# Kernel tuning notes

Measured on AMD Instinct MI355X. Metric: run time of the kernel, lower is better.

The kernel has to match this reference:

```python
import jax, jax.numpy as jnp
import numpy as np

B, N, DIM = 4, 16384, 256
H, D, G = 8, 64, 32  # heads, dim_head, slice_num; inner = H*D = 512


def setup_inputs() -> dict:
    key = jax.random.key(0)
    ks = jax.random.split(key, 12)
    inner = H * D
    s = lambda fan_in: 1.0 / np.sqrt(fan_in)
    inp = {
        "x": jax.random.normal(ks[0], (B, N, DIM), jnp.float32),
        # weights stored (in, out) so forward is x @ W + b
        "Wfx": jax.random.uniform(ks[1], (DIM, inner), jnp.float32, -s(DIM), s(DIM)),
        "bfx": jnp.zeros((inner,), jnp.float32),
        "Wx": jax.random.uniform(ks[2], (DIM, inner), jnp.float32, -s(DIM), s(DIM)),
        "bx": jnp.zeros((inner,), jnp.float32),
        "Wslice": jnp.linalg.qr(jax.random.normal(ks[3], (D, G), jnp.float32))[0],  # orthogonal init
        "bslice": jnp.zeros((G,), jnp.float32),
        "temperature": jnp.full((1, H, 1, 1), 0.5, jnp.float32),
        "Wq": jax.random.uniform(ks[4], (D, D), jnp.float32, -s(D), s(D)),
        "Wk": jax.random.uniform(ks[5], (D, D), jnp.float32, -s(D), s(D)),
        "Wv": jax.random.uniform(ks[6], (D, D), jnp.float32, -s(D), s(D)),
        "Wout": jax.random.uniform(ks[7], (inner, DIM), jnp.float32, -s(inner), s(inner)),
        "bout": jnp.zeros((DIM,), jnp.float32),
    }
    return inp


def reference(x, Wfx, bfx, Wx, bx, Wslice, bslice, temperature, Wq, Wk, Wv, Wout, bout):
    b, n, _ = x.shape
    # projections -> [B, H, N, D]
    fx_mid = (x @ Wfx + bfx).reshape(b, n, H, D).transpose(0, 2, 1, 3)
    x_mid = (x @ Wx + bx).reshape(b, n, H, D).transpose(0, 2, 1, 3)
    # soft slice assignment: [B, H, N, G]
    slice_logits = (x_mid @ Wslice + bslice) / temperature
    slice_weights = jax.nn.softmax(slice_logits, axis=-1)
    slice_norm = slice_weights.sum(axis=2)  # [B, H, G]
    # soft pooling to G slice tokens: [B, H, G, D]
    slice_token = jnp.einsum("bhnd,bhng->bhgd", fx_mid, slice_weights)
    slice_token = slice_token / (slice_norm[..., None] + 1e-5)
    # tiny attention over G tokens
    q = slice_token @ Wq
    k = slice_token @ Wk
    v = slice_token @ Wv
    scores = jnp.einsum("bhgd,bhkd->bhgk", q, k) / jnp.sqrt(jnp.asarray(D, q.dtype))
    attn = jax.nn.softmax(scores, axis=-1)
    out_slice = jnp.einsum("bhgk,bhkd->bhgd", attn, v)
    # scatter back to N points: [B, H, N, D] -> [B, N, H*D]
    out_x = jnp.einsum("bhgd,bhng->bhnd", out_slice, slice_weights)
    out_x = out_x.transpose(0, 2, 1, 3).reshape(b, n, H * D)
    return out_x @ Wout + bout
```

## Files before the change

### kernel.cpp

```cpp
#include <hip/hip_runtime.h>


typedef unsigned short u16;
typedef __attribute__((ext_vector_type(8))) unsigned short ushort8v;
typedef __attribute__((ext_vector_type(4))) unsigned short ushort4v;
typedef __attribute__((ext_vector_type(8))) short short8v;
typedef __attribute__((ext_vector_type(4))) float f32x4;

constexpr int Nc = 16384;
constexpr int BNc = 65536;

__device__ inline float b2f(u16 v) {
    union { unsigned int u; float f; } t; t.u = ((unsigned int)v) << 16; return t.f;
}
__device__ inline u16 f2b(float f) {
    union { float f; unsigned int u; } t; t.f = f;
    unsigned int u = t.u;
    return (u16)((u + 0x7fffu + ((u >> 16) & 1u)) >> 16);
}

__global__ __launch_bounds__(256) void k0_fold(
    const float* __restrict__ Wx, const float* __restrict__ Wslice,
    const float* __restrict__ bx, const float* __restrict__ bslice,
    u16* __restrict__ WxsT, float* __restrict__ bxs)
{
    int blk = blockIdx.x, tid = threadIdx.x;
    int h = tid >> 5, g = tid & 31;
    if (blk < 256) {
        int k = blk;
        float acc = 0.f;
        for (int d = 0; d < 64; d++)
            acc += Wx[k * 512 + h * 64 + d] * Wslice[d * 32 + g];
        WxsT[tid * 256 + k] = f2b(acc);
    } else {
        float acc = 0.f;
        for (int d = 0; d < 64; d++)
            acc += bx[h * 64 + d] * Wslice[d * 32 + g];
        bxs[tid] = acc + bslice[g];
    }
}

__global__ __launch_bounds__(256) void kprep_wfx(const float* __restrict__ Wfx,
                                                 u16* __restrict__ WfxT)
{
    int n = blockIdx.x, k = threadIdx.x;
    WfxT[n * 256 + k] = f2b(Wfx[k * 512 + n]);
}

template <int MODE, int NT>
__global__ __launch_bounds__(256, 2) void kgemm(
    const void* __restrict__ Ap, const u16* __restrict__ Bt,
    const float* __restrict__ bias, const float* __restrict__ temp,
    void* __restrict__ O1, u16* __restrict__ O2)
{
    constexpr int Kd = 256;
    __shared__ u16 Asl[4][64][8];
    __shared__ u16 Bsl[NT * 16][4][8];
    int tid = threadIdx.x;
    int wave = tid >> 6, lane = tid & 63;
    int lm = lane & 15, quad = lane >> 4;
    int row0 = blockIdx.x * 64;
    int sm = tid >> 2, skb = tid & 3;
    const u16* BtB = Bt;
    if (MODE == 2) BtB += (size_t)(row0 >> 14) * 65536;
    f32x4 acc[NT] = {};

    for (int k0 = 0; k0 < Kd; k0 += 32) {
        if (MODE < 2) {
            const float* A32 = (const float*)Ap;
            const f32x4* src = (const f32x4*)(A32 + (size_t)(row0 + sm) * Kd + k0 + skb * 8);
            f32x4 v0 = src[0], v1 = src[1];
            ushort8v o;
#pragma unroll
            for (int j = 0; j < 4; j++) { o[j] = f2b(v0[j]); o[4 + j] = f2b(v1[j]); }
            *(ushort8v*)&Asl[skb][sm][0] = o;
        } else {
            const u16* A16 = (const u16*)Ap;
            *(ushort8v*)&Asl[skb][sm][0] =
                *(const ushort8v*)(A16 + (size_t)(row0 + sm) * Kd + k0 + skb * 8);
        }
#pragma unroll
        for (int i = 0; i < NT / 4; i++) {
            int e = i * 256 + tid;
            int sn = e >> 2, sk = e & 3;
            *(ushort8v*)&Bsl[sn][sk][0] =
                *(const ushort8v*)(BtB + (size_t)sn * Kd + k0 + sk * 8);
        }
        __syncthreads();
        short8v af = *(short8v*)&Asl[quad][wave * 16 + lm][0];
#pragma unroll
        for (int nt = 0; nt < NT; nt++) {
            short8v bf = *(short8v*)&Bsl[nt * 16 + lm][quad][0];
            acc[nt] = __builtin_amdgcn_mfma_f32_16x16x32_bf16(af, bf, acc[nt], 0, 0, 0);
        }
        __syncthreads();
    }

    if (MODE == 0) {
        u16* fxT = (u16*)O1;
        int nbase = row0 + wave * 16 + quad * 4;
#pragma unroll
        for (int nt = 0; nt < NT; nt++) {
            int c = nt * 16 + lm;
            float bv = bias[c];
            ushort4v o;
#pragma unroll
            for (int r = 0; r < 4; r++) o[r] = f2b(acc[nt][r] + bv);
            *(ushort4v*)(fxT + (size_t)c * 65536 + nbase) = o;
        }
    } else if (MODE == 1) {
        int b = row0 >> 14;
        int nlbase = (row0 & 16383) + wave * 16 + quad * 4;
        u16* swb = (u16*)O1;
#pragma unroll
        for (int h = 0; h < 8; h++) {
            float it = 1.0f / temp[h];
            float bv0 = bias[h * 32 + lm];
            float bv1 = bias[h * 32 + 16 + lm];
            ushort4v p0, p1;
#pragma unroll
            for (int r = 0; r < 4; r++) {
                float v0 = (acc[2 * h][r] + bv0) * it;
                float v1 = (acc[2 * h + 1][r] + bv1) * it;
                float m = fmaxf(v0, v1);
                m = fmaxf(m, __shfl_xor(m, 1));
                m = fmaxf(m, __shfl_xor(m, 2));
                m = fmaxf(m, __shfl_xor(m, 4));
                m = fmaxf(m, __shfl_xor(m, 8));
                float e0 = __expf(v0 - m), e1 = __expf(v1 - m);
                float s = e0 + e1;
                s += __shfl_xor(s, 1);
                s += __shfl_xor(s, 2);
                s += __shfl_xor(s, 4);
                s += __shfl_xor(s, 8);
                float rs = 1.0f / s;
                float w0 = e0 * rs, w1 = e1 * rs;
                int row = row0 + wave * 16 + quad * 4 + r;
                swb[(size_t)row * 256 + h * 32 + lm] = f2b(w0);
                swb[(size_t)row * 256 + h * 32 + 16 + lm] = f2b(w1);
                p0[r] = f2b(w0); p1[r] = f2b(w1);
            }
            size_t gbase = (size_t)((b * 8 + h) * 32);
            *(ushort4v*)(O2 + (gbase + lm) * 16384 + nlbase) = p0;
            *(ushort4v*)(O2 + (gbase + 16 + lm) * 16384 + nlbase) = p1;
        }
    } else {
        float* out = (float*)O1;
#pragma unroll
        for (int nt = 0; nt < NT; nt++) {
            int c = nt * 16 + lm;
            float bv = bias[c];
#pragma unroll
            for (int r = 0; r < 4; r++)
                out[(size_t)(row0 + wave * 16 + quad * 4 + r) * 256 + c] = acc[nt][r] + bv;
        }
    }
}

__global__ __launch_bounds__(256) void k4_token_mfma(
    const u16* __restrict__ swT, const u16* __restrict__ fxT,
    float* __restrict__ token_part, float* __restrict__ norm_part)
{
    int bh = blockIdx.x, ky = blockIdx.y;
    int b = bh >> 3, h = bh & 7;
    int tid = threadIdx.x, wave = tid >> 6, lane = tid & 63;
    int lm = lane & 15, quad = lane >> 4;
    int mt = wave & 1, dp = wave >> 1;
    const u16* Ar = swT + ((size_t)(bh * 32 + mt * 16 + lm)) * 16384 + ky * 512 + quad * 8;
    const u16* Br0 = fxT + ((size_t)(h * 64 + dp * 32 + lm)) * 65536
                     + (size_t)b * 16384 + ky * 512 + quad * 8;
    const u16* Br1 = Br0 + (size_t)16 * 65536;
    f32x4 acc0 = {}, acc1 = {};
    float nacc = 0.f;
#pragma unroll
    for (int kk = 0; kk < 16; kk++) {
        short8v af = *(const short8v*)(Ar + kk * 32);
        short8v b0 = *(const short8v*)(Br0 + kk * 32);
        short8v b1 = *(const short8v*)(Br1 + kk * 32);
        acc0 = __builtin_amdgcn_mfma_f32_16x16x32_bf16(af, b0, acc0, 0, 0, 0);
        acc1 = __builtin_amdgcn_mfma_f32_16x16x32_bf16(af, b1, acc1, 0, 0, 0);
        if (dp == 0) {
            ushort8v au = (ushort8v&)af;
#pragma unroll
            for (int j = 0; j < 8; j++) nacc += b2f(au[j]);
        }
    }
    float* tp = token_part + ((size_t)(ky * 32 + bh)) * 2048;
#pragma unroll
    for (int r = 0; r < 4; r++) {
        int g = mt * 16 + quad * 4 + r;
        tp[g * 64 + dp * 32 + lm] = acc0[r];
        tp[g * 64 + dp * 32 + 16 + lm] = acc1[r];
    }
    if (dp == 0) {
        nacc += __shfl_xor(nacc, 16);
        nacc += __shfl_xor(nacc, 32);
        if (lane < 16)
            norm_part[(ky * 32 + bh) * 32 + mt * 16 + lm] = nacc;
    }
}

__global__ __launch_bounds__(256) void k4b_reduce(
    const float* __restrict__ tp, const float* __restrict__ np,
    float* __restrict__ tl)
{
    int t = blockIdx.x * 256 + threadIdx.x;
    int bh = t >> 11, e = t & 2047, g = e >> 6;
    float ts = 0.f, ns = 0.f;
    for (int ch = 0; ch < 32; ch++) {
        ts += tp[((size_t)(ch * 32 + bh)) * 2048 + e];
        ns += np[(ch * 32 + bh) * 32 + g];
    }
    tl[t] = ts / (ns + 1e-5f);
}

__global__ __launch_bounds__(256) void k5_attn(
    const float* __restrict__ tlg,
    const float* __restrict__ Wq, const float* __restrict__ Wk, const float* __restrict__ Wv,
    float* __restrict__ out_slice)
{
    __shared__ float tl[32][64];
    __shared__ float ql[32][64], kl[32][64], vl[32][64];
    __shared__ float sl[32][33];
    int bh = blockIdx.x, tid = threadIdx.x;
    const float* tk = tlg + (size_t)bh * 2048;

#pragma unroll
    for (int j = 0; j < 8; j++) {
        int idx = j * 256 + tid;
        tl[idx >> 6][idx & 63] = tk[idx];
    }
    __syncthreads();
#pragma unroll
    for (int j = 0; j < 8; j++) {
        int idx = j * 256 + tid;
        int g = idx >> 6, d = idx & 63;
        float aq = 0.f, ak = 0.f, av = 0.f;
        for (int e = 0; e < 64; e++) {
            float t = tl[g][e];
            aq += t * Wq[e * 64 + d];
            ak += t * Wk[e * 64 + d];
            av += t * Wv[e * 64 + d];
        }
        ql[g][d] = aq; kl[g][d] = ak; vl[g][d] = av;
    }
    __syncthreads();
#pragma unroll
    for (int j = 0; j < 4; j++) {
        int idx = j * 256 + tid;
        int gq = idx >> 5, gk = idx & 31;
        float s = 0.f;
        for (int d = 0; d < 64; d++) s += ql[gq][d] * kl[gk][d];
        sl[gq][gk] = s * 0.125f;
    }
    __syncthreads();
    if (tid < 32) {
        float m = -1e30f;
        for (int k2 = 0; k2 < 32; k2++) m = fmaxf(m, sl[tid][k2]);
        float s = 0.f;
        for (int k2 = 0; k2 < 32; k2++) { float e = __expf(sl[tid][k2] - m); sl[tid][k2] = e; s += e; }
        float r = 1.0f / s;
        for (int k2 = 0; k2 < 32; k2++) sl[tid][k2] *= r;
    }
    __syncthreads();
#pragma unroll
    for (int j = 0; j < 8; j++) {
        int idx = j * 256 + tid;
        int g = idx >> 6, d = idx & 63;
        float a = 0.f;
        for (int k2 = 0; k2 < 32; k2++) a += sl[g][k2] * vl[k2][d];
        out_slice[(size_t)bh * 2048 + idx] = a;
    }
}

__global__ __launch_bounds__(256) void kZ(
    const float* __restrict__ os, const float* __restrict__ Wout,
    u16* __restrict__ ZT)
{
    int b = blockIdx.x, cb = blockIdx.y;
    int t = threadIdx.x;
    int c = cb * 16 + (t & 15), kq = t >> 4;
    for (int k = kq * 16; k < kq * 16 + 16; k++) {
        int h = k >> 5, g = k & 31;
        const float* osr = os + ((size_t)(b * 8 + h)) * 2048 + g * 64;
        float acc = 0.f;
        for (int d = 0; d < 64; d++)
            acc += osr[d] * Wout[(h * 64 + d) * 256 + c];
        ZT[(size_t)b * 65536 + c * 256 + k] = f2b(acc);
    }
}

extern "C" void kernel_launch(void* const* d_in, const int* in_sizes, int n_in,
                              void* d_out, int out_size, void* d_ws, size_t ws_size,
                              hipStream_t stream)
{
    const float* x      = (const float*)d_in[0];
    const float* Wfx    = (const float*)d_in[1];
    const float* bfx    = (const float*)d_in[2];
    const float* Wx     = (const float*)d_in[3];
    const float* bx     = (const float*)d_in[4];
    const float* Wslice = (const float*)d_in[5];
    const float* bslice = (const float*)d_in[6];
    const float* temp   = (const float*)d_in[7];
    const float* Wq     = (const float*)d_in[8];
    const float* Wk     = (const float*)d_in[9];
    const float* Wv     = (const float*)d_in[10];
    const float* Wout   = (const float*)d_in[11];
    const float* bout   = (const float*)d_in[12];

    char* ws = (char*)d_ws;
    size_t off = 0;
    auto alloc = [&](size_t bytes) {
        void* p = ws + off;
        off = (off + bytes + 255) & ~(size_t)255;
        return p;
    };
    u16*   fxT   = (u16*)  alloc((size_t)512 * BNc * 2);
    u16*   swb   = (u16*)  alloc((size_t)BNc * 256 * 2);
    u16*   swT   = (u16*)  alloc((size_t)1024 * Nc * 2);
    float* tp    = (float*)alloc((size_t)1024 * 2048 * 4);
    float* np    = (float*)alloc(32768 * 4);
    float* tl    = (float*)alloc(65536 * 4);
    float* osl   = (float*)alloc(65536 * 4);
    u16*   ZT    = (u16*)  alloc(4 * 65536 * 2);
    u16*   WfxT  = (u16*)  alloc(512 * 256 * 2);
    u16*   WxsT  = (u16*)  alloc(256 * 256 * 2);
    float* bxs   = (float*)alloc(256 * 4);

    k0_fold<<<257, 256, 0, stream>>>(Wx, Wslice, bx, bslice, WxsT, bxs);
    kprep_wfx<<<512, 256, 0, stream>>>(Wfx, WfxT);

    kgemm<0, 32><<<1024, 256, 0, stream>>>(x, WfxT, bfx, nullptr, fxT, nullptr);

    kgemm<1, 16><<<1024, 256, 0, stream>>>(x, WxsT, bxs, temp, swb, swT);

    k4_token_mfma<<<dim3(32, 32), 256, 0, stream>>>(swT, fxT, tp, np);
    k4b_reduce<<<256, 256, 0, stream>>>(tp, np, tl);
    k5_attn<<<32, 256, 0, stream>>>(tl, Wq, Wk, Wv, osl);
    kZ<<<dim3(4, 16), 256, 0, stream>>>(osl, Wout, ZT);

    kgemm<2, 16><<<1024, 256, 0, stream>>>(swb, ZT, bout, nullptr, d_out, nullptr);
}
```

Measured before the change: 351.8 us.

## Fuse fx and slice projections into one GEMM, drop LDS staging

Concatenates the Wfx and folded Wx·Wslice weights into one bf16 matrix. A single kernel now reads x once and computes both the fx projection and the slice-softmax weights, where two separate GEMMs each read x before. Both the projection and output GEMMs now load operand fragments straight from global memory into registers, prefetching the next A chunk and dropping shared-memory staging and the __syncthreads barriers. The cost is higher register pressure (24 accumulators per wave), uneven work between the two wave columns (one only writes fx, the other also does the softmax), and repeated uncoalesced B loads that now rely on cache.

```diff
diff --git a/kernel.cpp b/kernel.cpp
--- a/kernel.cpp
+++ b/kernel.cpp
@@ -47,81 +47,72 @@
     WfxT[n * 256 + k] = f2b(Wfx[k * 512 + n]);
 }
 
-template <int MODE, int NT>
-__global__ __launch_bounds__(256, 2) void kgemm(
-    const void* __restrict__ Ap, const u16* __restrict__ Bt,
-    const float* __restrict__ bias, const float* __restrict__ temp,
-    void* __restrict__ O1, u16* __restrict__ O2)
-{
-    constexpr int Kd = 256;
-    __shared__ u16 Asl[4][64][8];
-    __shared__ u16 Bsl[NT * 16][4][8];
+__global__ __launch_bounds__(256, 3) void kproj(
+    const float* __restrict__ x, const u16* __restrict__ Ball,
+    const float* __restrict__ bfx, const float* __restrict__ bxs,
+    const float* __restrict__ temp,
+    u16* __restrict__ fxT, u16* __restrict__ swb, u16* __restrict__ swT)
+{
     int tid = threadIdx.x;
     int wave = tid >> 6, lane = tid & 63;
     int lm = lane & 15, quad = lane >> 4;
-    int row0 = blockIdx.x * 64;
-    int sm = tid >> 2, skb = tid & 3;
-    const u16* BtB = Bt;
-    if (MODE == 2) BtB += (size_t)(row0 >> 14) * 65536;
-    f32x4 acc[NT] = {};
-
-    for (int k0 = 0; k0 < Kd; k0 += 32) {
-        if (MODE < 2) {
-            const float* A32 = (const float*)Ap;
-            const f32x4* src = (const f32x4*)(A32 + (size_t)(row0 + sm) * Kd + k0 + skb * 8);
-            f32x4 v0 = src[0], v1 = src[1];
-            ushort8v o;
-#pragma unroll
-            for (int j = 0; j < 4; j++) { o[j] = f2b(v0[j]); o[4 + j] = f2b(v1[j]); }
-            *(ushort8v*)&Asl[skb][sm][0] = o;
-        } else {
-            const u16* A16 = (const u16*)Ap;
-            *(ushort8v*)&Asl[skb][sm][0] =
-                *(const ushort8v*)(A16 + (size_t)(row0 + sm) * Kd + k0 + skb * 8);
-        }
-#pragma unroll
-        for (int i = 0; i < NT / 4; i++) {
-            int e = i * 256 + tid;
-            int sn = e >> 2, sk = e & 3;
-            *(ushort8v*)&Bsl[sn][sk][0] =
-                *(const ushort8v*)(BtB + (size_t)sn * Kd + k0 + sk * 8);
-        }
-        __syncthreads();
-        short8v af = *(short8v*)&Asl[quad][wave * 16 + lm][0];
-#pragma unroll
-        for (int nt = 0; nt < NT; nt++) {
-            short8v bf = *(short8v*)&Bsl[nt * 16 + lm][quad][0];
-            acc[nt] = __builtin_amdgcn_mfma_f32_16x16x32_bf16(af, bf, acc[nt], 0, 0, 0);
-        }
-        __syncthreads();
-    }
-
-    if (MODE == 0) {
-        u16* fxT = (u16*)O1;
-        int nbase = row0 + wave * 16 + quad * 4;
-#pragma unroll
-        for (int nt = 0; nt < NT; nt++) {
-            int c = nt * 16 + lm;
-            float bv = bias[c];
+    int wr = wave & 1, wc = wave >> 1;
+    int row0 = blockIdx.x * 32;
+    int arow = row0 + wr * 16 + lm;
+
+    const float* Aptr = x + (size_t)arow * 256 + quad * 8;
+    const u16*   Bl   = Ball + (size_t)(wc * 384 + lm) * 256 + quad * 8;
+
+    f32x4 acc[24] = {};
+
+    f32x4 a0 = *(const f32x4*)(Aptr);
+    f32x4 a1 = *(const f32x4*)(Aptr + 4);
+
+    for (int k0 = 0; k0 < 256; k0 += 32) {
+        ushort8v au;
+#pragma unroll
+        for (int j = 0; j < 4; j++) { au[j] = f2b(a0[j]); au[4 + j] = f2b(a1[j]); }
+        short8v af = (short8v&)au;
+        if (k0 < 224) {
+            a0 = *(const f32x4*)(Aptr + k0 + 32);
+            a1 = *(const f32x4*)(Aptr + k0 + 36);
+        }
+#pragma unroll
+        for (int j = 0; j < 24; j++) {
+            short8v bf = *(const short8v*)(Bl + (size_t)j * 4096 + k0);
+            acc[j] = __builtin_amdgcn_mfma_f32_16x16x32_bf16(af, bf, acc[j], 0, 0, 0);
+        }
+    }
+
+    int nbase = row0 + wr * 16 + quad * 4;
+    int nfx = wc ? 8 : 24;
+#pragma unroll
+    for (int j = 0; j < 24; j++) {
+        if (j < nfx) {
+            int c = (wc * 24 + j) * 16 + lm;
+            float bv = bfx[c];
             ushort4v o;
 #pragma unroll
-            for (int r = 0; r < 4; r++) o[r] = f2b(acc[nt][r] + bv);
+            for (int r = 0; r < 4; r++) o[r] = f2b(acc[j][r] + bv);
             *(ushort4v*)(fxT + (size_t)c * 65536 + nbase) = o;
         }
-    } else if (MODE == 1) {
+    }
+
+    if (wc == 1) {
         int b = row0 >> 14;
-        int nlbase = (row0 & 16383) + wave * 16 + quad * 4;
-        u16* swb = (u16*)O1;
+        int nlbase = (row0 & 16383) + wr * 16 + quad * 4;
 #pragma unroll
         for (int h = 0; h < 8; h++) {
             float it = 1.0f / temp[h];
-            float bv0 = bias[h * 32 + lm];
-            float bv1 = bias[h * 32 + 16 + lm];
+            float bv0 = bxs[h * 32 + lm];
+            float bv1 = bxs[h * 32 + 16 + lm];
+            f32x4 A0 = acc[8 + 2 * h];
+            f32x4 A1 = acc[9 + 2 * h];
             ushort4v p0, p1;
 #pragma unroll
             for (int r = 0; r < 4; r++) {
-                float v0 = (acc[2 * h][r] + bv0) * it;
-                float v1 = (acc[2 * h + 1][r] + bv1) * it;
+                float v0 = (A0[r] + bv0) * it;
+                float v1 = (A1[r] + bv1) * it;
                 float m = fmaxf(v0, v1);
                 m = fmaxf(m, __shfl_xor(m, 1));
                 m = fmaxf(m, __shfl_xor(m, 2));
@@ -135,25 +126,48 @@
                 s += __shfl_xor(s, 8);
                 float rs = 1.0f / s;
                 float w0 = e0 * rs, w1 = e1 * rs;
-                int row = row0 + wave * 16 + quad * 4 + r;
+                int row = row0 + wr * 16 + quad * 4 + r;
                 swb[(size_t)row * 256 + h * 32 + lm] = f2b(w0);
                 swb[(size_t)row * 256 + h * 32 + 16 + lm] = f2b(w1);
                 p0[r] = f2b(w0); p1[r] = f2b(w1);
             }
             size_t gbase = (size_t)((b * 8 + h) * 32);
-            *(ushort4v*)(O2 + (gbase + lm) * 16384 + nlbase) = p0;
-            *(ushort4v*)(O2 + (gbase + 16 + lm) * 16384 + nlbase) = p1;
-        }
-    } else {
-        float* out = (float*)O1;
-#pragma unroll
-        for (int nt = 0; nt < NT; nt++) {
-            int c = nt * 16 + lm;
-            float bv = bias[c];
-#pragma unroll
-            for (int r = 0; r < 4; r++)
-                out[(size_t)(row0 + wave * 16 + quad * 4 + r) * 256 + c] = acc[nt][r] + bv;
-        }
+            *(ushort4v*)(swT + (gbase + lm) * 16384 + nlbase) = p0;
+            *(ushort4v*)(swT + (gbase + 16 + lm) * 16384 + nlbase) = p1;
+        }
+    }
+}
+
+__global__ __launch_bounds__(256, 3) void kout(
+    const u16* __restrict__ swb, const u16* __restrict__ ZT,
+    const float* __restrict__ bout, float* __restrict__ out)
+{
+    int tid = threadIdx.x;
+    int wave = tid >> 6, lane = tid & 63;
+    int lm = lane & 15, quad = lane >> 4;
+    int row0 = blockIdx.x * 64;
+
+    const u16* Abase = swb + (size_t)(row0 + wave * 16 + lm) * 256 + quad * 8;
+    const u16* Bl    = ZT + (size_t)(row0 >> 14) * 65536 + (size_t)lm * 256 + quad * 8;
+
+    f32x4 acc[16] = {};
+    short8v af = *(const short8v*)(Abase);
+    for (int k0 = 0; k0 < 256; k0 += 32) {
+        short8v a_cur = af;
+        if (k0 < 224) af = *(const short8v*)(Abase + k0 + 32);
+#pragma unroll
+        for (int j = 0; j < 16; j++) {
+            short8v bf = *(const short8v*)(Bl + (size_t)j * 4096 + k0);
+            acc[j] = __builtin_amdgcn_mfma_f32_16x16x32_bf16(a_cur, bf, acc[j], 0, 0, 0);
+        }
+    }
+#pragma unroll
+    for (int j = 0; j < 16; j++) {
+        int c = j * 16 + lm;
+        float bv = bout[c];
+#pragma unroll
+        for (int r = 0; r < 4; r++)
+            out[(size_t)(row0 + wave * 16 + quad * 4 + r) * 256 + c] = acc[j][r] + bv;
     }
 }
 
@@ -323,21 +337,21 @@
     float* tl    = (float*)alloc(65536 * 4);
     float* osl   = (float*)alloc(65536 * 4);
     u16*   ZT    = (u16*)  alloc(4 * 65536 * 2);
-    u16*   WfxT  = (u16*)  alloc(512 * 256 * 2);
-    u16*   WxsT  = (u16*)  alloc(256 * 256 * 2);
+    u16*   Ball  = (u16*)  alloc((size_t)768 * 256 * 2);
     float* bxs   = (float*)alloc(256 * 4);
+
+    u16* WfxT = Ball;
+    u16* WxsT = Ball + (size_t)512 * 256;
 
     k0_fold<<<257, 256, 0, stream>>>(Wx, Wslice, bx, bslice, WxsT, bxs);
     kprep_wfx<<<512, 256, 0, stream>>>(Wfx, WfxT);
 
-    kgemm<0, 32><<<1024, 256, 0, stream>>>(x, WfxT, bfx, nullptr, fxT, nullptr);
-
-    kgemm<1, 16><<<1024, 256, 0, stream>>>(x, WxsT, bxs, temp, swb, swT);
+    kproj<<<2048, 256, 0, stream>>>(x, Ball, bfx, bxs, temp, fxT, swb, swT);
 
     k4_token_mfma<<<dim3(32, 32), 256, 0, stream>>>(swT, fxT, tp, np);
     k4b_reduce<<<256, 256, 0, stream>>>(tp, np, tl);
     k5_attn<<<32, 256, 0, stream>>>(tl, Wq, Wk, Wv, osl);
     kZ<<<dim3(4, 16), 256, 0, stream>>>(osl, Wout, ZT);
 
-    kgemm<2, 16><<<1024, 256, 0, stream>>>(swb, ZT, bout, nullptr, d_out, nullptr);
-}
+    kout<<<1024, 256, 0, stream>>>(swb, ZT, bout, (float*)d_out);
+}
```

Result: slower. 523.0 us (+48.7%).
